# Kernel tuning notes

Measured on AMD Instinct MI355X. Metric: run time of the kernel, lower is better.

## Reference

```python
import jax, jax.numpy as jnp
import numpy as np

TW, NV, EMB, LAYERS = 25, 4, 128, 6
N, E = 65536, 262144
T_MAX = 16.0
EPS = 1e-5

def silu(x):
    return x * jax.nn.sigmoid(x)

def setup_inputs() -> dict:
    key = jax.random.key(0)
    ks = iter(jax.random.split(key, 32))
    def nrm(shape, scale=0.05):
        return jax.random.normal(next(ks), shape, jnp.float32) * scale
    inp = {}
    inp['x'] = jax.random.normal(next(ks), (N, TW), jnp.float32)
    inp['pos'] = jax.random.uniform(next(ks), (N, 1), jnp.float32)
    inp['variables'] = jax.random.uniform(next(ks), (N, NV), jnp.float32)
    inp['dt'] = jnp.full((1,), 0.1, jnp.float32)
    inp['edge_index'] = jax.random.randint(next(ks), (2, E), 0, N)
    inp['enc_W1'] = nrm((TW + NV + 1, EMB)); inp['enc_b1'] = jnp.zeros((EMB,), jnp.float32)
    inp['enc_W2'] = nrm((EMB, EMB));         inp['enc_b2'] = jnp.zeros((EMB,), jnp.float32)
    dmsg = 2 * EMB + TW + 1 + NV   # 286: x_i,x_j,u_i-u_j,pos_i-pos_j,vars_i
    dupd = 2 * EMB + NV            # 260: x, aggregated message, vars
    inp['msg_W1'] = nrm((LAYERS, dmsg, EMB)); inp['msg_b1'] = jnp.zeros((LAYERS, EMB), jnp.float32)
    inp['msg_W2'] = nrm((LAYERS, EMB, EMB));  inp['msg_b2'] = jnp.zeros((LAYERS, EMB), jnp.float32)
    inp['upd_W1'] = nrm((LAYERS, dupd, EMB)); inp['upd_b1'] = jnp.zeros((LAYERS, EMB), jnp.float32)
    inp['upd_W2'] = nrm((LAYERS, EMB, EMB));  inp['upd_b2'] = jnp.zeros((LAYERS, EMB), jnp.float32)
    inp['dec_W1'] = nrm((8, 1, 16)); inp['dec_b1'] = jnp.zeros((8,), jnp.float32)
    inp['dec_W2'] = nrm((1, 8, 14)); inp['dec_b2'] = jnp.zeros((1,), jnp.float32)
    return inp

def reference(x, pos, variables, dt, edge_index,
              enc_W1, enc_b1, enc_W2, enc_b2,
              msg_W1, msg_b1, msg_W2, msg_b2,
              upd_W1, upd_b1, upd_W2, upd_b2,
              dec_W1, dec_b1, dec_W2, dec_b2):
    vars3 = variables[:, :3]              # alpha, beta, gamma
    t = variables[:, 3:4] / T_MAX         # normalized time
    p = pos / jnp.max(pos)                # graph.pos /= pos.max()
    inp0 = jnp.concatenate([x, p, t, vars3], axis=-1)  # [N, 30]
    h = silu(silu(inp0 @ enc_W1 + enc_b1) @ enc_W2 + enc_b2)  # [N, EMB]

    src, dst = edge_index[0], edge_index[1]  # x_j = src, x_i = dst (source_to_target)
    deg = jax.ops.segment_sum(jnp.ones((E,), jnp.float32), dst, num_segments=N)
    inv_deg = (1.0 / jnp.maximum(deg, 1.0))[:, None]

    for l in range(LAYERS):
        m_in = jnp.concatenate(
            [h[dst], h[src], x[dst] - x[src], p[dst] - p[src], variables[dst]], axis=-1)
        m = silu(m_in @ msg_W1[l] + msg_b1[l])
        m = silu(m @ msg_W2[l] + msg_b2[l])                      # [E, EMB]
        agg = jax.ops.segment_sum(m, dst, num_segments=N) * inv_deg  # mean aggr
        u = silu(jnp.concatenate([h, agg, variables], axis=-1) @ upd_W1[l] + upd_b1[l])
        u = silu(u @ upd_W2[l] + upd_b2[l])
        h_new = h + u  # in_features == out_features -> residual
        # PyG InstanceNorm (affine=False), single graph (batch all zeros)
        mu = jnp.mean(h_new, axis=0, keepdims=True)
        var = jnp.var(h_new, axis=0, keepdims=True)
        h = (h_new - mu) * jax.lax.rsqrt(var + EPS)

    # decoder: Conv1d(1->8, k=16, s=3) -> SiLU -> Conv1d(8->1, k=14, s=1)
    z = h[:, None, :]  # [N, 1, EMB]
    z = jax.lax.conv_general_dilated(z, dec_W1, (3,), 'VALID',
                                     dimension_numbers=('NCH', 'OIH', 'NCH')) + dec_b1[None, :, None]
    z = silu(z)
    z = jax.lax.conv_general_dilated(z, dec_W2, (1,), 'VALID',
                                     dimension_numbers=('NCH', 'OIH', 'NCH')) + dec_b2[None, :, None]
    diff = z[:, 0, :]  # [N, TW]
    dtc = dt[0] * jnp.arange(1, TW + 1, dtype=jnp.float32)  # cumsum of dt*ones
    return jnp.tile(x[:, -1:], (1, TW)) + dtc[None, :] * diff
```

## Files before the change

### kernel.cpp

```cpp
#include <hip/hip_runtime.h>
#include <math.h>

#define N_NODES 65536
#define N_EDGES 262144
#define N_LAYERS 6
#define T_MAX_F 16.0f
#define EPS_F 1e-5f

typedef float  f32x4  __attribute__((ext_vector_type(4)));
typedef __bf16 bf16x8 __attribute__((ext_vector_type(8)));

__device__ __forceinline__ float silu_f(float v){
    return v / (1.0f + __expf(-v));
}

__device__ __forceinline__ f32x4 mfma16(bf16x8 a, bf16x8 b, f32x4 c){
    return __builtin_amdgcn_mfma_f32_16x16x32_bf16(a, b, c, 0, 0, 0);
}

#define PK_RA (6 * 20480)
#define PK_RB (6 * 20480)
#define PK_M2 (6 * 16384)
#define PK_U1 (6 * 36864)
#define PK_U2 (6 * 16384)
#define PK_TOTAL (PK_RA + PK_RB + PK_M2 + PK_U1 + PK_U2)

__global__ __launch_bounds__(256) void k_pack(const float* __restrict__ msgW1, const float* __restrict__ msgW2,
                                              const float* __restrict__ updW1, const float* __restrict__ updW2,
                                              __bf16* __restrict__ out){
    int pg = blockIdx.x * 256 + threadIdx.x;
    if (pg >= PK_TOTAL) return;
    int p = pg;
    int mode; const float* W; int perL;
    if (p < PK_RA){ mode = 0; W = msgW1; perL = 20480; }
    else if ((p -= PK_RA) < PK_RB){ mode = 1; W = msgW1; perL = 20480; }
    else if ((p -= PK_RB) < PK_M2){ mode = 2; W = msgW2; perL = 16384; }
    else if ((p -= PK_M2) < PK_U1){ mode = 3; W = updW1; perL = 36864; }
    else { p -= PK_U1; mode = 4; W = updW2; perL = 16384; }
    int l = p / perL, q = p % perL;
    int elem = q & 7, lane = (q >> 3) & 63, cb = (q >> 9) & 7, kb = q >> 12;
    int col = cb * 16 + (lane & 15);
    int k = kb * 32 + ((lane >> 4) << 3) + elem;
    float v = 0.0f;
    if (mode == 0){
        int r = -1;
        if (k < 128) r = k;
        else if (k < 153) r = 256 + (k - 128);
        else if (k == 153) r = 281;
        else if (k < 158) r = 282 + (k - 154);
        if (r >= 0) v = W[(size_t)l * 286 * 128 + (size_t)r * 128 + col];
    } else if (mode == 1){
        if (k < 128) v = W[(size_t)l * 286 * 128 + (size_t)(128 + k) * 128 + col];
        else if (k < 153) v = -W[(size_t)l * 286 * 128 + (size_t)(256 + (k - 128)) * 128 + col];
        else if (k == 153) v = -W[(size_t)l * 286 * 128 + (size_t)281 * 128 + col];
    } else {
        int Kreal = (mode == 3) ? 260 : 128;
        if (k < Kreal) v = W[(size_t)l * Kreal * 128 + (size_t)k * 128 + col];
    }
    out[pg] = (__bf16)v;
}

__global__ __launch_bounds__(256) void k_deg_max(const int* __restrict__ dst, const float* __restrict__ pos,
                                                 int* __restrict__ deg, unsigned* __restrict__ outmax){
    __shared__ float s[256];
    int tid = threadIdx.x;
    int e = blockIdx.x * 256 + tid;
    if (e < N_EDGES) atomicAdd(deg + dst[e], 1);
    if (blockIdx.x < N_NODES / 256){
        s[tid] = pos[blockIdx.x * 256 + tid];
        __syncthreads();
        for (int off = 128; off > 0; off >>= 1){
            if (tid < off) s[tid] = fmaxf(s[tid], s[tid + off]);
            __syncthreads();
        }
        if (tid == 0) atomicMax(outmax, __float_as_uint(s[0]));
    }
}

__global__ __launch_bounds__(256) void k_scan1(const int* __restrict__ deg, int* __restrict__ csum){
    __shared__ int s[256];
    int c = blockIdx.x, t = threadIdx.x;
    s[t] = deg[c * 256 + t];
    __syncthreads();
    for (int o = 128; o > 0; o >>= 1){ if (t < o) s[t] += s[t + o]; __syncthreads(); }
    if (t == 0) csum[c] = s[0];
}

__global__ __launch_bounds__(256) void k_scan2(const int* __restrict__ csum, int* __restrict__ coff){
    __shared__ int s[256];
    int t = threadIdx.x;
    s[t] = csum[t];
    __syncthreads();
    for (int o = 1; o < 256; o <<= 1){
        int v = (t >= o) ? s[t - o] : 0;
        __syncthreads();
        s[t] += v;
        __syncthreads();
    }
    coff[t] = s[t] - csum[t];
}

__global__ __launch_bounds__(256) void k_scan3(const int* __restrict__ deg, const int* __restrict__ coff,
                                               int* __restrict__ cursor){
    __shared__ int s[256];
    int c = blockIdx.x, t = threadIdx.x;
    int d = deg[c * 256 + t];
    s[t] = d;
    __syncthreads();
    for (int o = 1; o < 256; o <<= 1){
        int v = (t >= o) ? s[t - o] : 0;
        __syncthreads();
        s[t] += v;
        __syncthreads();
    }
    cursor[c * 256 + t] = coff[c] + s[t] - d;
}

__global__ __launch_bounds__(256) void k_scatter_prep(const int* __restrict__ esrc, const int* __restrict__ edst,
                                                      int* __restrict__ cursor,
                                                      int* __restrict__ ssrcS, int* __restrict__ sdstS,
                                                      const float* __restrict__ pos, const unsigned* __restrict__ maxp,
                                                      const int* __restrict__ deg,
                                                      float* __restrict__ p, float* __restrict__ invdeg){
    int e = blockIdx.x * 256 + threadIdx.x;
    if (e < N_EDGES){
        int d = edst[e];
        int slot = atomicAdd(cursor + d, 1);
        ssrcS[slot] = esrc[e];
        sdstS[slot] = d;
    }
    if (blockIdx.x < N_NODES / 256){
        int i = blockIdx.x * 256 + threadIdx.x;
        float mp = __uint_as_float(*maxp);
        p[i] = pos[i] / mp;
        invdeg[i] = 1.0f / fmaxf((float)deg[i], 1.0f);
    }
}

__device__ __forceinline__ void gemm44(const float* A, int lda, const float* __restrict__ W,
                                       int kq_begin, int kq_end, int r0, int c0, float acc[4][4]){
    for (int kq = kq_begin; kq < kq_end; ++kq){
        int k = kq * 4;
        float a[4][4], w[4][4];
        #pragma unroll
        for (int i = 0; i < 4; ++i){
            float4 v = *(const float4*)(A + (r0 + i) * lda + k);
            a[i][0] = v.x; a[i][1] = v.y; a[i][2] = v.z; a[i][3] = v.w;
        }
        #pragma unroll
        for (int kk = 0; kk < 4; ++kk){
            float4 v = *(const float4*)(W + (k + kk) * 128 + c0);
            w[kk][0] = v.x; w[kk][1] = v.y; w[kk][2] = v.z; w[kk][3] = v.w;
        }
        #pragma unroll
        for (int kk = 0; kk < 4; ++kk)
            #pragma unroll
            for (int i = 0; i < 4; ++i)
                #pragma unroll
                for (int j = 0; j < 4; ++j)
                    acc[i][j] = fmaf(a[i][kk], w[kk][j], acc[i][j]);
    }
}

__global__ __launch_bounds__(256) void k_enc(const float* __restrict__ x, const float* __restrict__ p,
                                             const float* __restrict__ vars,
                                             const float* __restrict__ W1, const float* __restrict__ b1,
                                             const float* __restrict__ W2, const float* __restrict__ b2,
                                             float* __restrict__ hA){
    __shared__ __align__(16) float sin_[32 * 32];
    __shared__ __align__(16) float sw1[32 * 128];
    __shared__ __align__(16) float sy[32 * 128];
    int tid = threadIdx.x;
    int n0 = blockIdx.x * 32;
    for (int i = tid; i < 32 * 32; i += 256){
        int e = i >> 5, k = i & 31;
        int node = n0 + e;
        float v;
        if (k < 25)       v = x[node * 25 + k];
        else if (k == 25) v = p[node];
        else if (k == 26) v = vars[node * 4 + 3] * (1.0f / T_MAX_F);
        else if (k < 30)  v = vars[node * 4 + (k - 27)];
        else              v = 0.0f;
        sin_[e * 32 + k] = v;
    }
    for (int i = tid; i < 32 * 128; i += 256){
        int r = i >> 7;
        sw1[i] = (r < 30) ? W1[i] : 0.0f;
    }
    __syncthreads();
    int c0 = (tid & 31) * 4, r0 = (tid >> 5) * 4;
    float acc[4][4] = {};
    gemm44(sin_, 32, sw1, 0, 8, r0, c0, acc);
    float4 bv = *(const float4*)(b1 + c0);
    float b_[4] = {bv.x, bv.y, bv.z, bv.w};
    #pragma unroll
    for (int i = 0; i < 4; ++i){
        float4 o;
        o.x = silu_f(acc[i][0] + b_[0]);
        o.y = silu_f(acc[i][1] + b_[1]);
        o.z = silu_f(acc[i][2] + b_[2]);
        o.w = silu_f(acc[i][3] + b_[3]);
        *(float4*)(sy + (r0 + i) * 128 + c0) = o;
    }
    __syncthreads();
    float acc2[4][4] = {};
    gemm44(sy, 128, W2, 0, 32, r0, c0, acc2);
    float4 b2v = *(const float4*)(b2 + c0);
    float bb[4] = {b2v.x, b2v.y, b2v.z, b2v.w};
    #pragma unroll
    for (int i = 0; i < 4; ++i){
        float4 o;
        o.x = silu_f(acc2[i][0] + bb[0]);
        o.y = silu_f(acc2[i][1] + bb[1]);
        o.z = silu_f(acc2[i][2] + bb[2]);
        o.w = silu_f(acc2[i][3] + bb[3]);
        *(float4*)(hA + (size_t)(n0 + r0 + i) * 128 + c0) = o;
    }
}

__global__ __launch_bounds__(256) void k_npre(const float* __restrict__ hA, const float* __restrict__ x,
                                              const float* __restrict__ p, const float* __restrict__ vars,
                                              const float* __restrict__ statPrev, int apply_ln,
                                              const __bf16* __restrict__ Wra, const __bf16* __restrict__ Wrb,
                                              const float* __restrict__ b1,
                                              __bf16* __restrict__ raO, __bf16* __restrict__ rbO,
                                              float* __restrict__ aggZ, float* __restrict__ statCurZ){
    __shared__ __align__(16) __bf16 sA[10 * 64 * 8];
    __shared__ __align__(16) float sOut[32 * 264];
    __shared__ __align__(16) float smu[128], sistd[128];
    int tid = threadIdx.x;
    int n0 = blockIdx.x * 32;
    if (apply_ln && tid < 128){
        float m = statPrev[tid] * (1.0f / N_NODES);
        float v = statPrev[128 + tid] * (1.0f / N_NODES) - m * m;
        smu[tid] = m;
        sistd[tid] = rsqrtf(v + EPS_F);
    }
    if (blockIdx.x == 0) statCurZ[tid] = 0.f;
    {
        float4 z4 = {0.f, 0.f, 0.f, 0.f};
        #pragma unroll
        for (int it = 0; it < 4; ++it){
            int i = tid + it * 256;
            int e = i >> 5, ch = i & 31;
            *(float4*)(aggZ + (size_t)(n0 + e) * 128 + ch * 4) = z4;
        }
    }
    __syncthreads();
    #pragma unroll
    for (int it = 0; it < 3; ++it){
        int j = tid + it * 256;
        if (j < 640){
            int f = j >> 6, lane = j & 63;
            int kb = f >> 1, mt = f & 1;
            int e = (lane & 15) + mt * 16, kh = lane >> 4;
            int node = n0 + e;
            bf16x8 o;
            if (kb < 4){
                int k0 = kb * 32 + kh * 8;
                float4 v0 = *(const float4*)(hA + (size_t)node * 128 + k0);
                float4 v1 = *(const float4*)(hA + (size_t)node * 128 + k0 + 4);
                if (apply_ln){
                    float4 m0 = *(const float4*)(smu + k0),   m1 = *(const float4*)(smu + k0 + 4);
                    float4 s0 = *(const float4*)(sistd + k0), s1 = *(const float4*)(sistd + k0 + 4);
                    v0.x = (v0.x - m0.x) * s0.x; v0.y = (v0.y - m0.y) * s0.y;
                    v0.z = (v0.z - m0.z) * s0.z; v0.w = (v0.w - m0.w) * s0.w;
                    v1.x = (v1.x - m1.x) * s1.x; v1.y = (v1.y - m1.y) * s1.y;
                    v1.z = (v1.z - m1.z) * s1.z; v1.w = (v1.w - m1.w) * s1.w;
                }
                o[0] = (__bf16)v0.x; o[1] = (__bf16)v0.y; o[2] = (__bf16)v0.z; o[3] = (__bf16)v0.w;
                o[4] = (__bf16)v1.x; o[5] = (__bf16)v1.y; o[6] = (__bf16)v1.z; o[7] = (__bf16)v1.w;
            } else {
                #pragma unroll
                for (int jj = 0; jj < 8; ++jj){
                    int fk = kh * 8 + jj;
                    float v;
                    if (fk < 25)       v = x[node * 25 + fk];
                    else if (fk == 25) v = p[node];
                    else if (fk < 30)  v = vars[node * 4 + (fk - 26)];
                    else               v = 0.0f;
                    o[jj] = (__bf16)v;
                }
            }
            *(bf16x8*)(sA + (f * 64 + lane) * 8) = o;
        }
    }
    __syncthreads();
    int w = tid >> 6, lane = tid & 63;
    int clo = lane & 15, rhi = lane >> 4;
    f32x4 z = {0.f, 0.f, 0.f, 0.f};
    f32x4 aR[2][2] = {{z, z}, {z, z}};
    f32x4 aB[2][2] = {{z, z}, {z, z}};
    #pragma unroll
    for (int kb = 0; kb < 5; ++kb){
        bf16x8 a0 = *(bf16x8*)(sA + ((kb * 2 + 0) * 64 + lane) * 8);
        bf16x8 a1 = *(bf16x8*)(sA + ((kb * 2 + 1) * 64 + lane) * 8);
        bf16x8 wr0 = *(const bf16x8*)(Wra + (size_t)((kb * 8 + 2 * w)     * 64 + lane) * 8);
        bf16x8 wr1 = *(const bf16x8*)(Wra + (size_t)((kb * 8 + 2 * w + 1) * 64 + lane) * 8);
        bf16x8 wb0 = *(const bf16x8*)(Wrb + (size_t)((kb * 8 + 2 * w)     * 64 + lane) * 8);
        bf16x8 wb1 = *(const bf16x8*)(Wrb + (size_t)((kb * 8 + 2 * w + 1) * 64 + lane) * 8);
        aR[0][0] = mfma16(a0, wr0, aR[0][0]);
        aR[0][1] = mfma16(a0, wr1, aR[0][1]);
        aR[1][0] = mfma16(a1, wr0, aR[1][0]);
        aR[1][1] = mfma16(a1, wr1, aR[1][1]);
        aB[0][0] = mfma16(a0, wb0, aB[0][0]);
        aB[0][1] = mfma16(a0, wb1, aB[0][1]);
        aB[1][0] = mfma16(a1, wb0, aB[1][0]);
        aB[1][1] = mfma16(a1, wb1, aB[1][1]);
    }
    #pragma unroll
    for (int nf = 0; nf < 2; ++nf){
        int col = (2 * w + nf) * 16 + clo;
        float bv = b1[col];
        #pragma unroll
        for (int mt = 0; mt < 2; ++mt)
            #pragma unroll
            for (int i = 0; i < 4; ++i){
                int e = mt * 16 + rhi * 4 + i;
                sOut[e * 264 + col]       = aR[mt][nf][i] + bv;
                sOut[e * 264 + 128 + col] = aB[mt][nf][i];
            }
    }
    __syncthreads();
    #pragma unroll
    for (int it = 0; it < 4; ++it){
        int j = tid + it * 256;
        int row = j >> 5, c8 = j & 31;
        const float* src = sOut + row * 264 + c8 * 8;
        bf16x8 o;
        #pragma unroll
        for (int t = 0; t < 8; ++t) o[t] = (__bf16)src[t];
        __bf16* dstp = (c8 < 16) ? (raO + (size_t)(n0 + row) * 128 + c8 * 8)
                                 : (rbO + (size_t)(n0 + row) * 128 + (c8 - 16) * 8);
        *(bf16x8*)dstp = o;
    }
}

__global__ __launch_bounds__(256) void k_edge3(const __bf16* __restrict__ ra, const __bf16* __restrict__ rb,
                                               const int* __restrict__ ssrcS, const int* __restrict__ sdstS,
                                               const __bf16* __restrict__ Wp2, const float* __restrict__ bias2,
                                               float* __restrict__ agg){
    __shared__ __align__(16) unsigned char smem[64 * 128 * 4];
    __shared__ int sd[64], ss[64];
    __bf16* sA   = (__bf16*)smem;
    float*  msum = (float*)smem;
    int tid = threadIdx.x;
    int e0 = blockIdx.x * 64;
    if (tid < 64){ sd[tid] = sdstS[e0 + tid]; ss[tid] = ssrcS[e0 + tid]; }
    __syncthreads();
    #pragma unroll
    for (int it = 0; it < 4; ++it){
        int j = tid + it * 256;
        int f = j >> 6, lane = j & 63;
        int kb = f >> 2, mt = f & 3;
        int e = (lane & 15) + mt * 16;
        int k0 = kb * 32 + (lane >> 4) * 8;
        bf16x8 va = *(const bf16x8*)(ra + (size_t)sd[e] * 128 + k0);
        bf16x8 vb = *(const bf16x8*)(rb + (size_t)ss[e] * 128 + k0);
        bf16x8 o;
        #pragma unroll
        for (int t = 0; t < 8; ++t)
            o[t] = (__bf16)silu_f((float)va[t] + (float)vb[t]);
        *(bf16x8*)(sA + (f * 64 + lane) * 8) = o;
    }
    __syncthreads();
    int w = tid >> 6, lane = tid & 63;
    int cb0 = 2 * w, clo = lane & 15, rhi = lane >> 4;
    f32x4 z = {0.f, 0.f, 0.f, 0.f};
    f32x4 acc[4][2] = {{z, z}, {z, z}, {z, z}, {z, z}};
    #pragma unroll
    for (int kb = 0; kb < 4; ++kb){
        bf16x8 a0 = *(bf16x8*)(sA + ((kb * 4 + 0) * 64 + lane) * 8);
        bf16x8 a1 = *(bf16x8*)(sA + ((kb * 4 + 1) * 64 + lane) * 8);
        bf16x8 a2 = *(bf16x8*)(sA + ((kb * 4 + 2) * 64 + lane) * 8);
        bf16x8 a3 = *(bf16x8*)(sA + ((kb * 4 + 3) * 64 + lane) * 8);
        bf16x8 w0 = *(const bf16x8*)(Wp2 + (size_t)((kb * 8 + cb0)     * 64 + lane) * 8);
        bf16x8 w1 = *(const bf16x8*)(Wp2 + (size_t)((kb * 8 + cb0 + 1) * 64 + lane) * 8);
        acc[0][0] = mfma16(a0, w0, acc[0][0]);
        acc[0][1] = mfma16(a0, w1, acc[0][1]);
        acc[1][0] = mfma16(a1, w0, acc[1][0]);
        acc[1][1] = mfma16(a1, w1, acc[1][1]);
        acc[2][0] = mfma16(a2, w0, acc[2][0]);
        acc[2][1] = mfma16(a2, w1, acc[2][1]);
        acc[3][0] = mfma16(a3, w0, acc[3][0]);
        acc[3][1] = mfma16(a3, w1, acc[3][1]);
    }
    __syncthreads();
    #pragma unroll
    for (int nf = 0; nf < 2; ++nf){
        int col = (cb0 + nf) * 16 + clo;
        float bv = bias2[col];
        #pragma unroll
        for (int mt = 0; mt < 4; ++mt)
            #pragma unroll
            for (int i = 0; i < 4; ++i){
                int row = mt * 16 + rhi * 4 + i;
                msum[row * 128 + col] = silu_f(acc[mt][nf][i] + bv);
            }
    }
    __syncthreads();
    int col = tid & 127, half = tid >> 7;
    int base = half * 32;
    float run = 0.0f;
    for (int r = 0; r < 32; ++r){
        int row = base + r;
        run += msum[row * 128 + col];
        bool flush = (r == 31) || (sd[row + 1] != sd[row]);
        if (flush){
            atomicAdd(agg + (size_t)sd[row] * 128 + col, run);
            run = 0.0f;
        }
    }
}

__global__ __launch_bounds__(256) void k_upd_m(float* __restrict__ hA, const float* __restrict__ agg,
                                               const float* __restrict__ vars, const float* __restrict__ invdeg,
                                               const float* __restrict__ statPrev, int apply_ln,
                                               const __bf16* __restrict__ Wp1, const float* __restrict__ bias1,
                                               const __bf16* __restrict__ Wp2, const float* __restrict__ bias2,
                                               float* __restrict__ statCur){
    __shared__ __align__(16) __bf16 sA1[36 * 64 * 8];
    __shared__ __align__(16) float smu[128], sistd[128];
    __bf16* zb = sA1;
    int tid = threadIdx.x;
    int n0 = blockIdx.x * 64;
    if (apply_ln && tid < 128){
        float m = statPrev[tid] * (1.0f / N_NODES);
        float v = statPrev[128 + tid] * (1.0f / N_NODES) - m * m;
        smu[tid] = m;
        sistd[tid] = rsqrtf(v + EPS_F);
    }
    __syncthreads();
    #pragma unroll
    for (int it = 0; it < 9; ++it){
        int idx = tid + it * 256;
        int f = idx >> 6, lane = idx & 63;
        int kb = f >> 2, mt = f & 3;
        int row = (lane & 15) + mt * 16;
        int node = n0 + row;
        int k0 = kb * 32 + ((lane >> 4) << 3);
        bf16x8 o;
        if (k0 < 128){
            float4 v0 = *(const float4*)(hA + (size_t)node * 128 + k0);
            float4 v1 = *(const float4*)(hA + (size_t)node * 128 + k0 + 4);
            if (apply_ln){
                float4 m0 = *(const float4*)(smu + k0),   m1 = *(const float4*)(smu + k0 + 4);
                float4 s0 = *(const float4*)(sistd + k0), s1 = *(const float4*)(sistd + k0 + 4);
                v0.x = (v0.x - m0.x) * s0.x; v0.y = (v0.y - m0.y) * s0.y;
                v0.z = (v0.z - m0.z) * s0.z; v0.w = (v0.w - m0.w) * s0.w;
                v1.x = (v1.x - m1.x) * s1.x; v1.y = (v1.y - m1.y) * s1.y;
                v1.z = (v1.z - m1.z) * s1.z; v1.w = (v1.w - m1.w) * s1.w;
            }
            o[0] = (__bf16)v0.x; o[1] = (__bf16)v0.y; o[2] = (__bf16)v0.z; o[3] = (__bf16)v0.w;
            o[4] = (__bf16)v1.x; o[5] = (__bf16)v1.y; o[6] = (__bf16)v1.z; o[7] = (__bf16)v1.w;
        } else if (k0 < 256){
            int g0 = k0 - 128;
            float4 v0 = *(const float4*)(agg + (size_t)node * 128 + g0);
            float4 v1 = *(const float4*)(agg + (size_t)node * 128 + g0 + 4);
            float s = invdeg[node];
            o[0] = (__bf16)(v0.x * s); o[1] = (__bf16)(v0.y * s); o[2] = (__bf16)(v0.z * s); o[3] = (__bf16)(v0.w * s);
            o[4] = (__bf16)(v1.x * s); o[5] = (__bf16)(v1.y * s); o[6] = (__bf16)(v1.z * s); o[7] = (__bf16)(v1.w * s);
        } else {
            int fk = k0 - 256;
            #pragma unroll
            for (int jj = 0; jj < 8; ++jj){
                int kk = fk + jj;
                o[jj] = (__bf16)((kk < 4) ? vars[(size_t)node * 4 + kk] : 0.0f);
            }
        }
        *(bf16x8*)(sA1 + (size_t)idx * 8) = o;
    }
    __syncthreads();
    int w = tid >> 6, lane = tid & 63;
    int cb0 = 2 * w, clo = lane & 15, rhi = lane >> 4;
    f32x4 z = {0.f, 0.f, 0.f, 0.f};
    f32x4 acc[4][2] = {{z, z}, {z, z}, {z, z}, {z, z}};
    #pragma unroll
    for (int kb = 0; kb < 9; ++kb){
        bf16x8 w0 = *(const bf16x8*)(Wp1 + (size_t)((kb * 8 + cb0)     * 64 + lane) * 8);
        bf16x8 w1 = *(const bf16x8*)(Wp1 + (size_t)((kb * 8 + cb0 + 1) * 64 + lane) * 8);
        #pragma unroll
        for (int mt = 0; mt < 4; ++mt){
            bf16x8 a = *(bf16x8*)(sA1 + ((kb * 4 + mt) * 64 + lane) * 8);
            acc[mt][0] = mfma16(a, w0, acc[mt][0]);
            acc[mt][1] = mfma16(a, w1, acc[mt][1]);
        }
    }
    __syncthreads();
    #pragma unroll
    for (int nf = 0; nf < 2; ++nf){
        int col = (cb0 + nf) * 16 + clo;
        float bv = bias1[col];
        #pragma unroll
        for (int mt = 0; mt < 4; ++mt)
            #pragma unroll
            for (int i = 0; i < 4; ++i){
                int row = mt * 16 + rhi * 4 + i;
                zb[row * 152 + col] = (__bf16)silu_f(acc[mt][nf][i] + bv);
            }
    }
    __syncthreads();
    f32x4 acc2[4][2] = {{z, z}, {z, z}, {z, z}, {z, z}};
    #pragma unroll
    for (int kb = 0; kb < 4; ++kb){
        bf16x8 w0 = *(const bf16x8*)(Wp2 + (size_t)((kb * 8 + cb0)     * 64 + lane) * 8);
        bf16x8 w1 = *(const bf16x8*)(Wp2 + (size_t)((kb * 8 + cb0 + 1) * 64 + lane) * 8);
        int k0 = kb * 32 + ((lane >> 4) << 3);
        #pragma unroll
        for (int mt = 0; mt < 4; ++mt){
            int row = (lane & 15) + mt * 16;
            bf16x8 a = *(bf16x8*)(zb + row * 152 + k0);
            acc2[mt][0] = mfma16(a, w0, acc2[mt][0]);
            acc2[mt][1] = mfma16(a, w1, acc2[mt][1]);
        }
    }
    float sm[2] = {0.f, 0.f}, sq[2] = {0.f, 0.f};
    #pragma unroll
    for (int nf = 0; nf < 2; ++nf){
        int col = (cb0 + nf) * 16 + clo;
        float bv = bias2[col];
        float muv = apply_ln ? smu[col] : 0.0f;
        float sdv = apply_ln ? sistd[col] : 1.0f;
        #pragma unroll
        for (int mt = 0; mt < 4; ++mt)
            #pragma unroll
            for (int i = 0; i < 4; ++i){
                int row = mt * 16 + rhi * 4 + i;
                size_t idx = (size_t)(n0 + row) * 128 + col;
                float u = silu_f(acc2[mt][nf][i] + bv);
                float hln = (hA[idx] - muv) * sdv;
                float hv = hln + u;
                hA[idx] = hv;
                sm[nf] += hv; sq[nf] += hv * hv;
            }
    }
    #pragma unroll
    for (int nf = 0; nf < 2; ++nf){
        float s = sm[nf], q = sq[nf];
        s += __shfl_xor(s, 16); q += __shfl_xor(q, 16);
        s += __shfl_xor(s, 32); q += __shfl_xor(q, 32);
        if (rhi == 0){
            int col = (cb0 + nf) * 16 + clo;
            atomicAdd(statCur + col, s);
            atomicAdd(statCur + 128 + col, q);
        }
    }
}

#define DECNB 16
__global__ __launch_bounds__(256) void k_dec(const float* __restrict__ h, const float* __restrict__ x,
                                             const float* __restrict__ dt,
                                             const float* __restrict__ W1, const float* __restrict__ b1,
                                             const float* __restrict__ W2, const float* __restrict__ b2,
                                             const float* __restrict__ statPrev,
                                             float* __restrict__ out){
    __shared__ __align__(16) float sh[DECNB * 132];
    __shared__ __align__(16) float so[DECNB * 312];
    __shared__ float pp[DECNB * 8 * 26];
    __shared__ float sw1[128], sw2[112], sb1[8];
    __shared__ __align__(16) float smu[128], sistd[128];
    int tid = threadIdx.x;
    int n0 = blockIdx.x * DECNB;
    if (tid < 128){
        float m = statPrev[tid] * (1.0f / N_NODES);
        float v = statPrev[128 + tid] * (1.0f / N_NODES) - m * m;
        smu[tid] = m;
        sistd[tid] = rsqrtf(v + EPS_F);
        sw1[tid] = W1[tid];
    } else if (tid < 240) sw2[tid - 128] = W2[tid - 128];
    if (tid < 8) sb1[tid] = b1[tid];
    __syncthreads();
    for (int i = tid; i < DECNB * 32; i += 256){
        int g = i >> 5, chunk = i & 31;
        float4 v = *(const float4*)(h + (size_t)(n0 + g) * 128 + chunk * 4);
        float4 m = *(const float4*)(smu + chunk * 4);
        float4 s = *(const float4*)(sistd + chunk * 4);
        v.x = (v.x - m.x) * s.x; v.y = (v.y - m.y) * s.y;
        v.z = (v.z - m.z) * s.z; v.w = (v.w - m.w) * s.w;
        *(float4*)(sh + g * 132 + chunk * 4) = v;
    }
    __syncthreads();
    {
        int g = tid >> 4, c = (tid >> 1) & 7, jh = tid & 1;
        int j0 = jh * 19;
        float w[16];
        #pragma unroll
        for (int k = 0; k < 16; ++k) w[k] = sw1[c * 16 + k];
        float bc = sb1[c];
        float win[16];
        #pragma unroll
        for (int k = 0; k < 16; ++k) win[k] = sh[g * 132 + 3 * j0 + k];
        #pragma unroll
        for (int j = 0; j < 19; ++j){
            float a = bc;
            #pragma unroll
            for (int k = 0; k < 16; ++k) a = fmaf(win[k], w[k], a);
            so[g * 312 + c * 38 + j0 + j] = silu_f(a);
            if (j < 18){
                #pragma unroll
                for (int k = 0; k < 13; ++k) win[k] = win[k + 3];
                int base = g * 132 + 3 * (j0 + j + 1) + 13;
                win[13] = sh[base]; win[14] = sh[base + 1]; win[15] = sh[base + 2];
            }
        }
    }
    __syncthreads();
    {
        int g = tid >> 4, c = (tid >> 1) & 7, th = tid & 1;
        int t0 = th * 13;
        int nt = th ? 12 : 13;
        float w[14];
        #pragma unroll
        for (int k = 0; k < 14; ++k) w[k] = sw2[c * 14 + k];
        float win[14];
        #pragma unroll
        for (int k = 0; k < 14; ++k) win[k] = so[g * 312 + c * 38 + t0 + k];
        #pragma unroll
        for (int t = 0; t < 13; ++t){
            if (t < nt){
                float a = 0.0f;
                #pragma unroll
                for (int k = 0; k < 14; ++k) a = fmaf(win[k], w[k], a);
                pp[(g * 8 + c) * 26 + t0 + t] = a;
            }
            if (t + 1 < nt){
                #pragma unroll
                for (int k = 0; k < 13; ++k) win[k] = win[k + 1];
                win[13] = so[g * 312 + c * 38 + t0 + t + 14];
            }
        }
    }
    __syncthreads();
    float dtv = dt[0];
    for (int i = tid; i < DECNB * 25; i += 256){
        int g = i / 25, t = i % 25;
        float a = b2[0];
        #pragma unroll
        for (int c = 0; c < 8; ++c) a += pp[(g * 8 + c) * 26 + t];
        out[(size_t)(n0 + g) * 25 + t] = x[(size_t)(n0 + g) * 25 + 24] + dtv * (float)(t + 1) * a;
    }
}

extern "C" void kernel_launch(void* const* d_in, const int* in_sizes, int n_in,
                              void* d_out, int out_size, void* d_ws, size_t ws_size,
                              hipStream_t stream){
    (void)in_sizes; (void)n_in; (void)out_size; (void)ws_size;
    const float* x      = (const float*)d_in[0];
    const float* pos    = (const float*)d_in[1];
    const float* vars   = (const float*)d_in[2];
    const float* dt     = (const float*)d_in[3];
    const int*   ei     = (const int*)d_in[4];
    const float* encW1  = (const float*)d_in[5];
    const float* encb1  = (const float*)d_in[6];
    const float* encW2  = (const float*)d_in[7];
    const float* encb2  = (const float*)d_in[8];
    const float* msgW1  = (const float*)d_in[9];
    const float* msgb1  = (const float*)d_in[10];
    const float* msgW2  = (const float*)d_in[11];
    const float* msgb2  = (const float*)d_in[12];
    const float* updW1  = (const float*)d_in[13];
    const float* updb1  = (const float*)d_in[14];
    const float* updW2  = (const float*)d_in[15];
    const float* updb2  = (const float*)d_in[16];
    const float* decW1  = (const float*)d_in[17];
    const float* decb1  = (const float*)d_in[18];
    const float* decW2  = (const float*)d_in[19];
    const float* decb2  = (const float*)d_in[20];
    float* out = (float*)d_out;

    float* ws = (float*)d_ws;
    size_t off = 0;
    float* hA      = ws + off; off += (size_t)N_NODES * 128;
    float* agg     = ws + off; off += (size_t)N_NODES * 128;
    float* sstat   = ws + off; off += 2 * 256;
    float* p       = ws + off; off += N_NODES;
    float* invdeg  = ws + off; off += N_NODES;
    int* deg       = (int*)(ws + off); off += N_NODES;
    unsigned* maxp = (unsigned*)(ws + off); off += 2;
    int* csum      = (int*)(ws + off); off += 256;
    int* coff      = (int*)(ws + off); off += 256;
    int* cursor    = (int*)(ws + off); off += N_NODES;
    int* ssrcS     = (int*)(ws + off); off += N_EDGES;
    int* sdstS     = (int*)(ws + off); off += N_EDGES;
    __bf16* wpack  = (__bf16*)(ws + off); off += (PK_TOTAL + 1) / 2;
    __bf16* raB    = (__bf16*)(ws + off); off += (size_t)N_NODES * 64;
    __bf16* rbB    = (__bf16*)(ws + off); off += (size_t)N_NODES * 64;

    __bf16* pra = wpack;
    __bf16* prb = pra + PK_RA;
    __bf16* pm2 = prb + PK_RB;
    __bf16* pu1 = pm2 + PK_M2;
    __bf16* pu2 = pu1 + PK_U1;

    const int* esrc = ei;
    const int* edst = ei + N_EDGES;

    hipMemsetAsync(deg, 0, (size_t)N_NODES * sizeof(int) + sizeof(unsigned), stream);

    k_pack<<<(PK_TOTAL + 255) / 256, 256, 0, stream>>>(msgW1, msgW2, updW1, updW2, wpack);
    k_deg_max<<<N_EDGES / 256, 256, 0, stream>>>(edst, pos, deg, maxp);
    k_scan1<<<256, 256, 0, stream>>>(deg, csum);
    k_scan2<<<1, 256, 0, stream>>>(csum, coff);
    k_scan3<<<256, 256, 0, stream>>>(deg, coff, cursor);
    k_scatter_prep<<<N_EDGES / 256, 256, 0, stream>>>(esrc, edst, cursor, ssrcS, sdstS,
                                                      pos, maxp, deg, p, invdeg);
    k_enc<<<N_NODES / 32, 256, 0, stream>>>(x, p, vars, encW1, encb1, encW2, encb2, hA);

    for (int l = 0; l < N_LAYERS; ++l){
        int cur = l & 1;
        float* statCur        = sstat + (size_t)cur * 256;
        const float* statPrev = sstat + (size_t)(cur ^ 1) * 256;
        k_npre<<<N_NODES / 32, 256, 0, stream>>>(hA, x, p, vars, statPrev, (l > 0) ? 1 : 0,
            pra + (size_t)l * 20480, prb + (size_t)l * 20480, msgb1 + l * 128,
            raB, rbB, agg, statCur);
        k_edge3<<<N_EDGES / 64, 256, 0, stream>>>(raB, rbB, ssrcS, sdstS,
            pm2 + (size_t)l * 16384, msgb2 + l * 128, agg);
        k_upd_m<<<N_NODES / 64, 256, 0, stream>>>(hA, agg, vars, invdeg, statPrev, (l > 0) ? 1 : 0,
            pu1 + (size_t)l * 36864, updb1 + l * 128,
            pu2 + (size_t)l * 16384, updb2 + l * 128, statCur);
    }

    k_dec<<<N_NODES / DECNB, 256, 0, stream>>>(hA, x, dt, decW1, decb1, decW2, decb2,
                                               sstat + 256, out);
}
```

Baseline: 878.5 us.

## Fuse edge message and node update into one CSR-driven layer kernel

Combines the per-edge message MLP kernel and the node update kernel into one kernel. Each block owns 32 destination nodes and walks their CSR edge range, taken from a new rowptr array. Messages are summed into a shared-memory aggregate instead of a global agg buffer, which removes the global float atomics, the zeroing pass and the agg round trip through memory. The encoder also streams W2 through shared memory in chunks. The trade-offs are unbalanced work across blocks when degrees vary, smaller update tiles that reuse weights less, and shared-memory atomics.

```diff
diff --git a/kernel.cpp b/kernel.cpp
--- a/kernel.cpp
+++ b/kernel.cpp
@@ -101,7 +101,7 @@
 }
 
 __global__ __launch_bounds__(256) void k_scan3(const int* __restrict__ deg, const int* __restrict__ coff,
-                                               int* __restrict__ cursor){
+                                               int* __restrict__ cursor, int* __restrict__ rowptr){
     __shared__ int s[256];
     int c = blockIdx.x, t = threadIdx.x;
     int d = deg[c * 256 + t];
@@ -113,7 +113,9 @@
         s[t] += v;
         __syncthreads();
     }
-    cursor[c * 256 + t] = coff[c] + s[t] - d;
+    int start = coff[c] + s[t] - d;
+    cursor[c * 256 + t] = start;
+    rowptr[c * 256 + t] = start;
 }
 
 __global__ __launch_bounds__(256) void k_scatter_prep(const int* __restrict__ esrc, const int* __restrict__ edst,
@@ -137,7 +139,7 @@
     }
 }
 
-__device__ __forceinline__ void gemm44(const float* A, int lda, const float* __restrict__ W,
+__device__ __forceinline__ void gemm44(const float* A, int lda, const float* W,
                                        int kq_begin, int kq_end, int r0, int c0, float acc[4][4]){
     for (int kq = kq_begin; kq < kq_end; ++kq){
         int k = kq * 4;
@@ -168,7 +170,7 @@
                                              const float* __restrict__ W2, const float* __restrict__ b2,
                                              float* __restrict__ hA){
     __shared__ __align__(16) float sin_[32 * 32];
-    __shared__ __align__(16) float sw1[32 * 128];
+    __shared__ __align__(16) float swA[32 * 128];
     __shared__ __align__(16) float sy[32 * 128];
     int tid = threadIdx.x;
     int n0 = blockIdx.x * 32;
@@ -185,26 +187,33 @@
     }
     for (int i = tid; i < 32 * 128; i += 256){
         int r = i >> 7;
-        sw1[i] = (r < 30) ? W1[i] : 0.0f;
+        swA[i] = (r < 30) ? W1[i] : 0.0f;
     }
     __syncthreads();
     int c0 = (tid & 31) * 4, r0 = (tid >> 5) * 4;
-    float acc[4][4] = {};
-    gemm44(sin_, 32, sw1, 0, 8, r0, c0, acc);
-    float4 bv = *(const float4*)(b1 + c0);
-    float b_[4] = {bv.x, bv.y, bv.z, bv.w};
-    #pragma unroll
-    for (int i = 0; i < 4; ++i){
-        float4 o;
-        o.x = silu_f(acc[i][0] + b_[0]);
-        o.y = silu_f(acc[i][1] + b_[1]);
-        o.z = silu_f(acc[i][2] + b_[2]);
-        o.w = silu_f(acc[i][3] + b_[3]);
-        *(float4*)(sy + (r0 + i) * 128 + c0) = o;
-    }
-    __syncthreads();
+    {
+        float acc[4][4] = {};
+        gemm44(sin_, 32, swA, 0, 8, r0, c0, acc);
+        float4 bv = *(const float4*)(b1 + c0);
+        float b_[4] = {bv.x, bv.y, bv.z, bv.w};
+        #pragma unroll
+        for (int i = 0; i < 4; ++i){
+            float4 o;
+            o.x = silu_f(acc[i][0] + b_[0]);
+            o.y = silu_f(acc[i][1] + b_[1]);
+            o.z = silu_f(acc[i][2] + b_[2]);
+            o.w = silu_f(acc[i][3] + b_[3]);
+            *(float4*)(sy + (r0 + i) * 128 + c0) = o;
+        }
+    }
     float acc2[4][4] = {};
-    gemm44(sy, 128, W2, 0, 32, r0, c0, acc2);
+    for (int c = 0; c < 4; ++c){
+        __syncthreads();
+        for (int i = tid; i < 1024; i += 256)
+            ((float4*)swA)[i] = ((const float4*)(W2 + (size_t)c * 32 * 128))[i];
+        __syncthreads();
+        gemm44(sy + c * 32, 128, swA, 0, 8, r0, c0, acc2);
+    }
     float4 b2v = *(const float4*)(b2 + c0);
     float bb[4] = {b2v.x, b2v.y, b2v.z, b2v.w};
     #pragma unroll
@@ -224,7 +233,7 @@
                                               const __bf16* __restrict__ Wra, const __bf16* __restrict__ Wrb,
                                               const float* __restrict__ b1,
                                               __bf16* __restrict__ raO, __bf16* __restrict__ rbO,
-                                              float* __restrict__ aggZ, float* __restrict__ statCurZ){
+                                              float* __restrict__ statCurZ){
     __shared__ __align__(16) __bf16 sA[10 * 64 * 8];
     __shared__ __align__(16) float sOut[32 * 264];
     __shared__ __align__(16) float smu[128], sistd[128];
@@ -237,15 +246,6 @@
         sistd[tid] = rsqrtf(v + EPS_F);
     }
     if (blockIdx.x == 0) statCurZ[tid] = 0.f;
-    {
-        float4 z4 = {0.f, 0.f, 0.f, 0.f};
-        #pragma unroll
-        for (int it = 0; it < 4; ++it){
-            int i = tid + it * 256;
-            int e = i >> 5, ch = i & 31;
-            *(float4*)(aggZ + (size_t)(n0 + e) * 128 + ch * 4) = z4;
-        }
-    }
     __syncthreads();
     #pragma unroll
     for (int it = 0; it < 3; ++it){
@@ -336,178 +336,189 @@
     }
 }
 
-__global__ __launch_bounds__(256) void k_edge3(const __bf16* __restrict__ ra, const __bf16* __restrict__ rb,
+__global__ __launch_bounds__(256) void k_layer(float* __restrict__ hA,
+                                               const __bf16* __restrict__ ra, const __bf16* __restrict__ rb,
                                                const int* __restrict__ ssrcS, const int* __restrict__ sdstS,
-                                               const __bf16* __restrict__ Wp2, const float* __restrict__ bias2,
-                                               float* __restrict__ agg){
-    __shared__ __align__(16) unsigned char smem[64 * 128 * 4];
-    __shared__ int sd[64], ss[64];
-    __bf16* sA   = (__bf16*)smem;
-    float*  msum = (float*)smem;
-    int tid = threadIdx.x;
-    int e0 = blockIdx.x * 64;
-    if (tid < 64){ sd[tid] = sdstS[e0 + tid]; ss[tid] = ssrcS[e0 + tid]; }
-    __syncthreads();
-    #pragma unroll
-    for (int it = 0; it < 4; ++it){
-        int j = tid + it * 256;
-        int f = j >> 6, lane = j & 63;
-        int kb = f >> 2, mt = f & 3;
-        int e = (lane & 15) + mt * 16;
-        int k0 = kb * 32 + (lane >> 4) * 8;
-        bf16x8 va = *(const bf16x8*)(ra + (size_t)sd[e] * 128 + k0);
-        bf16x8 vb = *(const bf16x8*)(rb + (size_t)ss[e] * 128 + k0);
-        bf16x8 o;
-        #pragma unroll
-        for (int t = 0; t < 8; ++t)
-            o[t] = (__bf16)silu_f((float)va[t] + (float)vb[t]);
-        *(bf16x8*)(sA + (f * 64 + lane) * 8) = o;
-    }
-    __syncthreads();
-    int w = tid >> 6, lane = tid & 63;
-    int cb0 = 2 * w, clo = lane & 15, rhi = lane >> 4;
-    f32x4 z = {0.f, 0.f, 0.f, 0.f};
-    f32x4 acc[4][2] = {{z, z}, {z, z}, {z, z}, {z, z}};
-    #pragma unroll
-    for (int kb = 0; kb < 4; ++kb){
-        bf16x8 a0 = *(bf16x8*)(sA + ((kb * 4 + 0) * 64 + lane) * 8);
-        bf16x8 a1 = *(bf16x8*)(sA + ((kb * 4 + 1) * 64 + lane) * 8);
-        bf16x8 a2 = *(bf16x8*)(sA + ((kb * 4 + 2) * 64 + lane) * 8);
-        bf16x8 a3 = *(bf16x8*)(sA + ((kb * 4 + 3) * 64 + lane) * 8);
-        bf16x8 w0 = *(const bf16x8*)(Wp2 + (size_t)((kb * 8 + cb0)     * 64 + lane) * 8);
-        bf16x8 w1 = *(const bf16x8*)(Wp2 + (size_t)((kb * 8 + cb0 + 1) * 64 + lane) * 8);
-        acc[0][0] = mfma16(a0, w0, acc[0][0]);
-        acc[0][1] = mfma16(a0, w1, acc[0][1]);
-        acc[1][0] = mfma16(a1, w0, acc[1][0]);
-        acc[1][1] = mfma16(a1, w1, acc[1][1]);
-        acc[2][0] = mfma16(a2, w0, acc[2][0]);
-        acc[2][1] = mfma16(a2, w1, acc[2][1]);
-        acc[3][0] = mfma16(a3, w0, acc[3][0]);
-        acc[3][1] = mfma16(a3, w1, acc[3][1]);
-    }
-    __syncthreads();
-    #pragma unroll
-    for (int nf = 0; nf < 2; ++nf){
-        int col = (cb0 + nf) * 16 + clo;
-        float bv = bias2[col];
-        #pragma unroll
-        for (int mt = 0; mt < 4; ++mt)
-            #pragma unroll
-            for (int i = 0; i < 4; ++i){
-                int row = mt * 16 + rhi * 4 + i;
-                msum[row * 128 + col] = silu_f(acc[mt][nf][i] + bv);
-            }
-    }
-    __syncthreads();
-    int col = tid & 127, half = tid >> 7;
-    int base = half * 32;
-    float run = 0.0f;
-    for (int r = 0; r < 32; ++r){
-        int row = base + r;
-        run += msum[row * 128 + col];
-        bool flush = (r == 31) || (sd[row + 1] != sd[row]);
-        if (flush){
-            atomicAdd(agg + (size_t)sd[row] * 128 + col, run);
-            run = 0.0f;
-        }
-    }
-}
-
-__global__ __launch_bounds__(256) void k_upd_m(float* __restrict__ hA, const float* __restrict__ agg,
+                                               const int* __restrict__ rowptr,
                                                const float* __restrict__ vars, const float* __restrict__ invdeg,
                                                const float* __restrict__ statPrev, int apply_ln,
-                                               const __bf16* __restrict__ Wp1, const float* __restrict__ bias1,
-                                               const __bf16* __restrict__ Wp2, const float* __restrict__ bias2,
+                                               const __bf16* __restrict__ Wm2, const float* __restrict__ mb2,
+                                               const __bf16* __restrict__ Wu1, const float* __restrict__ ub1,
+                                               const __bf16* __restrict__ Wu2, const float* __restrict__ ub2,
                                                float* __restrict__ statCur){
-    __shared__ __align__(16) __bf16 sA1[36 * 64 * 8];
+    __shared__ __align__(16) float aggL[32 * 128];
+    __shared__ __align__(16) __bf16 uFrag[18 * 64 * 8];
     __shared__ __align__(16) float smu[128], sistd[128];
-    __bf16* zb = sA1;
+    __shared__ int sd[64], ss[64];
+    __bf16* zb = (__bf16*)aggL;
+
     int tid = threadIdx.x;
-    int n0 = blockIdx.x * 64;
+    int n0 = blockIdx.x * 32;
     if (apply_ln && tid < 128){
         float m = statPrev[tid] * (1.0f / N_NODES);
         float v = statPrev[128 + tid] * (1.0f / N_NODES) - m * m;
         smu[tid] = m;
         sistd[tid] = rsqrtf(v + EPS_F);
     }
-    __syncthreads();
-    #pragma unroll
-    for (int it = 0; it < 9; ++it){
-        int idx = tid + it * 256;
-        int f = idx >> 6, lane = idx & 63;
-        int kb = f >> 2, mt = f & 3;
-        int row = (lane & 15) + mt * 16;
-        int node = n0 + row;
-        int k0 = kb * 32 + ((lane >> 4) << 3);
-        bf16x8 o;
-        if (k0 < 128){
-            float4 v0 = *(const float4*)(hA + (size_t)node * 128 + k0);
-            float4 v1 = *(const float4*)(hA + (size_t)node * 128 + k0 + 4);
-            if (apply_ln){
-                float4 m0 = *(const float4*)(smu + k0),   m1 = *(const float4*)(smu + k0 + 4);
-                float4 s0 = *(const float4*)(sistd + k0), s1 = *(const float4*)(sistd + k0 + 4);
-                v0.x = (v0.x - m0.x) * s0.x; v0.y = (v0.y - m0.y) * s0.y;
-                v0.z = (v0.z - m0.z) * s0.z; v0.w = (v0.w - m0.w) * s0.w;
-                v1.x = (v1.x - m1.x) * s1.x; v1.y = (v1.y - m1.y) * s1.y;
-                v1.z = (v1.z - m1.z) * s1.z; v1.w = (v1.w - m1.w) * s1.w;
-            }
-            o[0] = (__bf16)v0.x; o[1] = (__bf16)v0.y; o[2] = (__bf16)v0.z; o[3] = (__bf16)v0.w;
-            o[4] = (__bf16)v1.x; o[5] = (__bf16)v1.y; o[6] = (__bf16)v1.z; o[7] = (__bf16)v1.w;
-        } else if (k0 < 256){
-            int g0 = k0 - 128;
-            float4 v0 = *(const float4*)(agg + (size_t)node * 128 + g0);
-            float4 v1 = *(const float4*)(agg + (size_t)node * 128 + g0 + 4);
-            float s = invdeg[node];
-            o[0] = (__bf16)(v0.x * s); o[1] = (__bf16)(v0.y * s); o[2] = (__bf16)(v0.z * s); o[3] = (__bf16)(v0.w * s);
-            o[4] = (__bf16)(v1.x * s); o[5] = (__bf16)(v1.y * s); o[6] = (__bf16)(v1.z * s); o[7] = (__bf16)(v1.w * s);
-        } else {
-            int fk = k0 - 256;
-            #pragma unroll
-            for (int jj = 0; jj < 8; ++jj){
-                int kk = fk + jj;
-                o[jj] = (__bf16)((kk < 4) ? vars[(size_t)node * 4 + kk] : 0.0f);
-            }
-        }
-        *(bf16x8*)(sA1 + (size_t)idx * 8) = o;
-    }
-    __syncthreads();
+    {
+        float4 z4 = {0.f, 0.f, 0.f, 0.f};
+        #pragma unroll
+        for (int it = 0; it < 4; ++it)
+            ((float4*)aggL)[tid + it * 256] = z4;
+    }
+
     int w = tid >> 6, lane = tid & 63;
     int cb0 = 2 * w, clo = lane & 15, rhi = lane >> 4;
     f32x4 z = {0.f, 0.f, 0.f, 0.f};
-    f32x4 acc[4][2] = {{z, z}, {z, z}, {z, z}, {z, z}};
+
+    int eBeg = rowptr[n0];
+    int eEnd = (n0 + 32 < N_NODES) ? rowptr[n0 + 32] : N_EDGES;
+
+    for (int eb = eBeg; eb < eEnd; eb += 64){
+        int cnt = eEnd - eb; if (cnt > 64) cnt = 64;
+        __syncthreads();
+        if (tid < 64){
+            sd[tid] = (tid < cnt) ? sdstS[eb + tid] : -1;
+            ss[tid] = (tid < cnt) ? ssrcS[eb + tid] : 0;
+        }
+        __syncthreads();
+        __bf16* sE = uFrag;
+        #pragma unroll
+        for (int it = 0; it < 4; ++it){
+            int j = tid + it * 256;
+            int f = j >> 6, ln = j & 63;
+            int kb = f >> 2, mt = f & 3;
+            int er = (ln & 15) + mt * 16;
+            int k0 = kb * 32 + (ln >> 4) * 8;
+            bf16x8 o;
+            if (er < cnt){
+                bf16x8 va = *(const bf16x8*)(ra + (size_t)sd[er] * 128 + k0);
+                bf16x8 vb = *(const bf16x8*)(rb + (size_t)ss[er] * 128 + k0);
+                #pragma unroll
+                for (int t = 0; t < 8; ++t)
+                    o[t] = (__bf16)silu_f((float)va[t] + (float)vb[t]);
+            } else {
+                #pragma unroll
+                for (int t = 0; t < 8; ++t) o[t] = (__bf16)0.f;
+            }
+            *(bf16x8*)(sE + (f * 64 + ln) * 8) = o;
+        }
+        __syncthreads();
+        f32x4 acc[4][2] = {{z, z}, {z, z}, {z, z}, {z, z}};
+        #pragma unroll
+        for (int kb = 0; kb < 4; ++kb){
+            bf16x8 w0 = *(const bf16x8*)(Wm2 + (size_t)((kb * 8 + cb0)     * 64 + lane) * 8);
+            bf16x8 w1 = *(const bf16x8*)(Wm2 + (size_t)((kb * 8 + cb0 + 1) * 64 + lane) * 8);
+            #pragma unroll
+            for (int mt = 0; mt < 4; ++mt){
+                bf16x8 a = *(bf16x8*)(sE + ((kb * 4 + mt) * 64 + lane) * 8);
+                acc[mt][0] = mfma16(a, w0, acc[mt][0]);
+                acc[mt][1] = mfma16(a, w1, acc[mt][1]);
+            }
+        }
+        #pragma unroll
+        for (int nf = 0; nf < 2; ++nf){
+            int col = (cb0 + nf) * 16 + clo;
+            float bv = mb2[col];
+            #pragma unroll
+            for (int mt = 0; mt < 4; ++mt){
+                float run = 0.f; int prev = -1;
+                #pragma unroll
+                for (int i = 0; i < 4; ++i){
+                    int er = mt * 16 + rhi * 4 + i;
+                    int d = sd[er];
+                    if (d >= 0){
+                        float mval = silu_f(acc[mt][nf][i] + bv);
+                        if (d != prev){
+                            if (prev >= 0) atomicAdd(aggL + (prev - n0) * 128 + col, run);
+                            run = 0.f; prev = d;
+                        }
+                        run += mval;
+                    }
+                }
+                if (prev >= 0) atomicAdd(aggL + (prev - n0) * 128 + col, run);
+            }
+        }
+    }
+    __syncthreads();
+
+    __bf16* sA1 = uFrag;
+    #pragma unroll
+    for (int it = 0; it < 5; ++it){
+        int idx = tid + it * 256;
+        if (idx < 1152){
+            int f = idx >> 6, ln = idx & 63;
+            int kb = f >> 1, mt = f & 1;
+            int row = (ln & 15) + mt * 16;
+            int node = n0 + row;
+            int k0 = kb * 32 + ((ln >> 4) << 3);
+            bf16x8 o;
+            if (k0 < 128){
+                float4 v0 = *(const float4*)(hA + (size_t)node * 128 + k0);
+                float4 v1 = *(const float4*)(hA + (size_t)node * 128 + k0 + 4);
+                if (apply_ln){
+                    float4 m0 = *(const float4*)(smu + k0),   m1 = *(const float4*)(smu + k0 + 4);
+                    float4 s0 = *(const float4*)(sistd + k0), s1 = *(const float4*)(sistd + k0 + 4);
+                    v0.x = (v0.x - m0.x) * s0.x; v0.y = (v0.y - m0.y) * s0.y;
+                    v0.z = (v0.z - m0.z) * s0.z; v0.w = (v0.w - m0.w) * s0.w;
+                    v1.x = (v1.x - m1.x) * s1.x; v1.y = (v1.y - m1.y) * s1.y;
+                    v1.z = (v1.z - m1.z) * s1.z; v1.w = (v1.w - m1.w) * s1.w;
+                }
+                o[0] = (__bf16)v0.x; o[1] = (__bf16)v0.y; o[2] = (__bf16)v0.z; o[3] = (__bf16)v0.w;
+                o[4] = (__bf16)v1.x; o[5] = (__bf16)v1.y; o[6] = (__bf16)v1.z; o[7] = (__bf16)v1.w;
+            } else if (k0 < 256){
+                int g0 = k0 - 128;
+                float4 v0 = *(const float4*)(aggL + row * 128 + g0);
+                float4 v1 = *(const float4*)(aggL + row * 128 + g0 + 4);
+                float s = invdeg[node];
+                o[0] = (__bf16)(v0.x * s); o[1] = (__bf16)(v0.y * s); o[2] = (__bf16)(v0.z * s); o[3] = (__bf16)(v0.w * s);
+                o[4] = (__bf16)(v1.x * s); o[5] = (__bf16)(v1.y * s); o[6] = (__bf16)(v1.z * s); o[7] = (__bf16)(v1.w * s);
+            } else {
+                int fk = k0 - 256;
+                #pragma unroll
+                for (int jj = 0; jj < 8; ++jj){
+                    int kk = fk + jj;
+                    o[jj] = (__bf16)((kk < 4) ? vars[(size_t)node * 4 + kk] : 0.0f);
+                }
+            }
+            *(bf16x8*)(sA1 + (size_t)idx * 8) = o;
+        }
+    }
+    __syncthreads();
+    f32x4 acc1[2][2] = {{z, z}, {z, z}};
     #pragma unroll
     for (int kb = 0; kb < 9; ++kb){
-        bf16x8 w0 = *(const bf16x8*)(Wp1 + (size_t)((kb * 8 + cb0)     * 64 + lane) * 8);
-        bf16x8 w1 = *(const bf16x8*)(Wp1 + (size_t)((kb * 8 + cb0 + 1) * 64 + lane) * 8);
-        #pragma unroll
-        for (int mt = 0; mt < 4; ++mt){
-            bf16x8 a = *(bf16x8*)(sA1 + ((kb * 4 + mt) * 64 + lane) * 8);
-            acc[mt][0] = mfma16(a, w0, acc[mt][0]);
-            acc[mt][1] = mfma16(a, w1, acc[mt][1]);
-        }
+        bf16x8 w0 = *(const bf16x8*)(Wu1 + (size_t)((kb * 8 + cb0)     * 64 + lane) * 8);
+        bf16x8 w1 = *(const bf16x8*)(Wu1 + (size_t)((kb * 8 + cb0 + 1) * 64 + lane) * 8);
+        bf16x8 a0 = *(bf16x8*)(sA1 + ((kb * 2 + 0) * 64 + lane) * 8);
+        bf16x8 a1 = *(bf16x8*)(sA1 + ((kb * 2 + 1) * 64 + lane) * 8);
+        acc1[0][0] = mfma16(a0, w0, acc1[0][0]);
+        acc1[0][1] = mfma16(a0, w1, acc1[0][1]);
+        acc1[1][0] = mfma16(a1, w0, acc1[1][0]);
+        acc1[1][1] = mfma16(a1, w1, acc1[1][1]);
     }
     __syncthreads();
     #pragma unroll
     for (int nf = 0; nf < 2; ++nf){
         int col = (cb0 + nf) * 16 + clo;
-        float bv = bias1[col];
-        #pragma unroll
-        for (int mt = 0; mt < 4; ++mt)
+        float bv = ub1[col];
+        #pragma unroll
+        for (int mt = 0; mt < 2; ++mt)
             #pragma unroll
             for (int i = 0; i < 4; ++i){
                 int row = mt * 16 + rhi * 4 + i;
-                zb[row * 152 + col] = (__bf16)silu_f(acc[mt][nf][i] + bv);
-            }
-    }
-    __syncthreads();
-    f32x4 acc2[4][2] = {{z, z}, {z, z}, {z, z}, {z, z}};
+                zb[row * 152 + col] = (__bf16)silu_f(acc1[mt][nf][i] + bv);
+            }
+    }
+    __syncthreads();
+    f32x4 acc2[2][2] = {{z, z}, {z, z}};
     #pragma unroll
     for (int kb = 0; kb < 4; ++kb){
-        bf16x8 w0 = *(const bf16x8*)(Wp2 + (size_t)((kb * 8 + cb0)     * 64 + lane) * 8);
-        bf16x8 w1 = *(const bf16x8*)(Wp2 + (size_t)((kb * 8 + cb0 + 1) * 64 + lane) * 8);
+        bf16x8 w0 = *(const bf16x8*)(Wu2 + (size_t)((kb * 8 + cb0)     * 64 + lane) * 8);
+        bf16x8 w1 = *(const bf16x8*)(Wu2 + (size_t)((kb * 8 + cb0 + 1) * 64 + lane) * 8);
         int k0 = kb * 32 + ((lane >> 4) << 3);
         #pragma unroll
-        for (int mt = 0; mt < 4; ++mt){
+        for (int mt = 0; mt < 2; ++mt){
             int row = (lane & 15) + mt * 16;
             bf16x8 a = *(bf16x8*)(zb + row * 152 + k0);
             acc2[mt][0] = mfma16(a, w0, acc2[mt][0]);
@@ -518,11 +529,11 @@
     #pragma unroll
     for (int nf = 0; nf < 2; ++nf){
         int col = (cb0 + nf) * 16 + clo;
-        float bv = bias2[col];
+        float bv = ub2[col];
         float muv = apply_ln ? smu[col] : 0.0f;
         float sdv = apply_ln ? sistd[col] : 1.0f;
         #pragma unroll
-        for (int mt = 0; mt < 4; ++mt)
+        for (int mt = 0; mt < 2; ++mt)
             #pragma unroll
             for (int i = 0; i < 4; ++i){
                 int row = mt * 16 + rhi * 4 + i;
@@ -671,7 +682,6 @@
     float* ws = (float*)d_ws;
     size_t off = 0;
     float* hA      = ws + off; off += (size_t)N_NODES * 128;
-    float* agg     = ws + off; off += (size_t)N_NODES * 128;
     float* sstat   = ws + off; off += 2 * 256;
     float* p       = ws + off; off += N_NODES;
     float* invdeg  = ws + off; off += N_NODES;
@@ -680,6 +690,7 @@
     int* csum      = (int*)(ws + off); off += 256;
     int* coff      = (int*)(ws + off); off += 256;
     int* cursor    = (int*)(ws + off); off += N_NODES;
+    int* rowptr    = (int*)(ws + off); off += N_NODES;
     int* ssrcS     = (int*)(ws + off); off += N_EDGES;
     int* sdstS     = (int*)(ws + off); off += N_EDGES;
     __bf16* wpack  = (__bf16*)(ws + off); off += (PK_TOTAL + 1) / 2;
@@ -701,7 +712,7 @@
     k_deg_max<<<N_EDGES / 256, 256, 0, stream>>>(edst, pos, deg, maxp);
     k_scan1<<<256, 256, 0, stream>>>(deg, csum);
     k_scan2<<<1, 256, 0, stream>>>(csum, coff);
-    k_scan3<<<256, 256, 0, stream>>>(deg, coff, cursor);
+    k_scan3<<<256, 256, 0, stream>>>(deg, coff, cursor, rowptr);
     k_scatter_prep<<<N_EDGES / 256, 256, 0, stream>>>(esrc, edst, cursor, ssrcS, sdstS,
                                                       pos, maxp, deg, p, invdeg);
     k_enc<<<N_NODES / 32, 256, 0, stream>>>(x, p, vars, encW1, encb1, encW2, encb2, hA);
@@ -712,10 +723,10 @@
         const float* statPrev = sstat + (size_t)(cur ^ 1) * 256;
         k_npre<<<N_NODES / 32, 256, 0, stream>>>(hA, x, p, vars, statPrev, (l > 0) ? 1 : 0,
             pra + (size_t)l * 20480, prb + (size_t)l * 20480, msgb1 + l * 128,
-            raB, rbB, agg, statCur);
-        k_edge3<<<N_EDGES / 64, 256, 0, stream>>>(raB, rbB, ssrcS, sdstS,
-            pm2 + (size_t)l * 16384, msgb2 + l * 128, agg);
-        k_upd_m<<<N_NODES / 64, 256, 0, stream>>>(hA, agg, vars, invdeg, statPrev, (l > 0) ? 1 : 0,
+            raB, rbB, statCur);
+        k_layer<<<N_NODES / 32, 256, 0, stream>>>(hA, raB, rbB, ssrcS, sdstS, rowptr,
+            vars, invdeg, statPrev, (l > 0) ? 1 : 0,
+            pm2 + (size_t)l * 16384, msgb2 + l * 128,
             pu1 + (size_t)l * 36864, updb1 + l * 128,
             pu2 + (size_t)l * 16384, updb2 + l * 128, statCur);
     }
```

Result: slower. 1.079 ms (+22.8%).
